# Kernel tuning notes

Hardware: AMD Instinct MI355X
Metric: run time of the kernel (lower is better)

The kernel has to match this reference:

```python
import jax, jax.numpy as jnp
import numpy as np
import math

B, S, D, H = 1, 2048, 2048, 16
DH = D // H  # 128
HALF = DH // 2  # 64


def setup_inputs() -> dict:
    key = jax.random.key(0)
    ks = jax.random.split(key, 6)
    x = jax.random.normal(ks[0], (B, S, D), dtype=jnp.float32)
    # rotary frequencies: freqs_cis = exp(i * t * theta), theta_j = 10000^{-2j/DH}
    inv_freq = 1.0 / (10000.0 ** (np.arange(0, DH, 2, dtype=np.float32) / DH))  # [HALF]
    t = np.arange(S, dtype=np.float32)
    angles = np.outer(t, inv_freq)  # [S, HALF]
    freqs_cos = jnp.asarray(np.cos(angles), dtype=jnp.float32)
    freqs_sin = jnp.asarray(np.sin(angles), dtype=jnp.float32)
    # additive causal mask [1,1,S,S]
    mask = jnp.triu(jnp.full((S, S), -1e9, dtype=jnp.float32), k=1)[None, None]
    scale = 0.02
    wq = jax.random.normal(ks[1], (D, D), dtype=jnp.float32) * scale
    wk = jax.random.normal(ks[2], (D, D), dtype=jnp.float32) * scale
    wv = jax.random.normal(ks[3], (D, D), dtype=jnp.float32) * scale
    wo = jax.random.normal(ks[4], (D, D), dtype=jnp.float32) * scale
    return {"x": x, "freqs_cos": freqs_cos, "freqs_sin": freqs_sin, "mask": mask,
            "wq": wq, "wk": wk, "wv": wv, "wo": wo, "start_pos": 0}


def _apply_rope(t, cos, sin):
    # t: [B,S,H,DH]; cos/sin: [S,HALF] broadcast as [1,S,1,HALF]
    tr = t.reshape(*t.shape[:-1], HALF, 2)
    even, odd = tr[..., 0], tr[..., 1]
    c = cos[None, :, None, :]
    s = sin[None, :, None, :]
    out_even = even * c - odd * s
    out_odd = even * s + odd * c
    return jnp.stack([out_even, out_odd], axis=-1).reshape(t.shape)


def reference(x, freqs_cos, freqs_sin, mask, wq, wk, wv, wo, start_pos):
    bsz, seqlen, _ = x.shape
    q = (x @ wq.T).reshape(bsz, seqlen, H, DH)
    k = (x @ wk.T).reshape(bsz, seqlen, H, DH)
    v = (x @ wv.T).reshape(bsz, seqlen, H, DH)
    q = _apply_rope(q, freqs_cos, freqs_sin)
    k = _apply_rope(k, freqs_cos, freqs_sin)
    q = q.transpose(0, 2, 1, 3)  # [B,H,S,DH]
    k = k.transpose(0, 2, 1, 3)
    v = v.transpose(0, 2, 1, 3)
    scores = jnp.einsum('bhqd,bhkd->bhqk', q, k) / math.sqrt(DH) + mask
    probs = jax.nn.softmax(scores, axis=-1)
    out = jnp.einsum('bhqk,bhkd->bhqd', probs, v)  # [B,H,S,DH]
    # faithful to original: transpose(2,3) then view(bsz, seqlen, dim)
    out = out.transpose(0, 1, 3, 2).reshape(bsz, seqlen, D)
    return out @ wo.T
```

## Files before the change

kernel.cpp:

```cpp
#include <hip/hip_runtime.h>

typedef unsigned short u16;
typedef unsigned int   u32;
typedef short  short8   __attribute__((ext_vector_type(8)));
typedef float  floatx4  __attribute__((ext_vector_type(4)));
typedef u16    ushortx2 __attribute__((ext_vector_type(2)));
typedef u16    ushortx4 __attribute__((ext_vector_type(4)));

__device__ __forceinline__ float bf2f(u16 u) {
  union { u32 i; float f; } v; v.i = ((u32)u) << 16; return v.f;
}
__device__ __forceinline__ u16 f2bf(float x) {
  union { float f; u32 i; } v; v.f = x;
  u32 r = v.i + 0x7FFFu + ((v.i >> 16) & 1u);
  return (u16)(r >> 16);
}

#if __has_builtin(__builtin_amdgcn_exp2f)
#define EXP2F(x) __builtin_amdgcn_exp2f(x)
#else
#define EXP2F(x) __exp2f(x)
#endif

#define GLOAD_LDS16(gptr, lptr)                                                   \
  __builtin_amdgcn_global_load_lds(                                               \
      (const __attribute__((address_space(1))) void*)(gptr),                      \
      (__attribute__((address_space(3))) void*)(lptr), 16, 0, 0)

__global__ __launch_bounds__(256) void cvt_all(
    const floatx4* __restrict__ x,  const floatx4* __restrict__ wq,
    const floatx4* __restrict__ wk, const floatx4* __restrict__ wv,
    const floatx4* __restrict__ wo,
    ushortx4* __restrict__ xb, ushortx4* __restrict__ wqkv,
    ushortx4* __restrict__ wob) {
  int i = blockIdx.x * 256 + threadIdx.x;
  const floatx4* in; ushortx4* out;
  switch (blockIdx.y) {
    case 0:  in = x;  out = xb; break;
    case 1:  in = wq; out = wqkv; break;
    case 2:  in = wk; out = wqkv + (size_t)1048576; break;
    case 3:  in = wv; out = wqkv + (size_t)2097152; break;
    default: in = wo; out = wob; break;
  }
  floatx4 v = in[i];
  ushortx4 o;
  o.x = f2bf(v.x); o.y = f2bf(v.y); o.z = f2bf(v.z); o.w = f2bf(v.w);
  out[i] = o;
}

__global__ __launch_bounds__(256) void gemm_bt(
    const u16* __restrict__ A, const u16* __restrict__ B, void* __restrict__ Cv,
    int M, int N, int K, int lda, int ldb, int ldc,
    long batchA, long batchB, long batchC, int outBF16) {
  const int m0 = blockIdx.y << 7;
  const int n0 = blockIdx.x << 7;

  A += (long)blockIdx.z * batchA;
  B += (long)blockIdx.z * batchB;
  const long cbase = (long)blockIdx.z * batchC;

  __shared__ __align__(16) u16 As[128][64];
  __shared__ __align__(16) u16 Bs[128][64];

  const int t = threadIdx.x;
  const int lane = t & 63;
  const int wave = t >> 6;
  const int wm = (wave >> 1) << 6;
  const int wn = (wave & 1) << 6;
  const int quad = lane >> 4;
  const int mrow = lane & 15;
  const int sw8 = mrow & 7;

  floatx4 acc[4][4] = {};

  const int srow = lane >> 3;
  const int gseg = (((lane & 7) ^ srow) << 3);
  const u16* gA = A + (long)(m0 + (wave << 5) + srow) * lda + gseg;
  const u16* gB = B + (long)(n0 + (wave << 5) + srow) * ldb + gseg;

  for (int k0 = 0; k0 < K; k0 += 64) {
    __syncthreads();
#pragma unroll
    for (int ii = 0; ii < 4; ii++) {
      GLOAD_LDS16(gA + k0 + (size_t)(ii << 3) * lda, &As[(wave << 5) + (ii << 3)][0]);
      GLOAD_LDS16(gB + k0 + (size_t)(ii << 3) * ldb, &Bs[(wave << 5) + (ii << 3)][0]);
    }
    __syncthreads();

#pragma unroll
    for (int kh = 0; kh < 2; kh++) {
      const int sidx = ((kh << 2) | quad) ^ sw8;
      short8 af[4], bfr[4];
#pragma unroll
      for (int i = 0; i < 4; i++)
        af[i] = *(const short8*)&As[wm + (i << 4) + mrow][sidx << 3];
#pragma unroll
      for (int j = 0; j < 4; j++)
        bfr[j] = *(const short8*)&Bs[wn + (j << 4) + mrow][sidx << 3];
#pragma unroll
      for (int i = 0; i < 4; i++)
#pragma unroll
        for (int j = 0; j < 4; j++)
          acc[i][j] = __builtin_amdgcn_mfma_f32_16x16x32_bf16(af[i], bfr[j], acc[i][j], 0, 0, 0);
    }
  }

#pragma unroll
  for (int i = 0; i < 4; i++) {
    int row0 = m0 + wm + (i << 4) + (quad << 2);
#pragma unroll
    for (int j = 0; j < 4; j++) {
      int col = n0 + wn + (j << 4) + mrow;
#pragma unroll
      for (int r = 0; r < 4; r++) {
        long idx = cbase + (long)(row0 + r) * ldc + col;
        float val = acc[i][j][r];
        if (outBF16) ((u16*)Cv)[idx] = f2bf(val);
        else         ((float*)Cv)[idx] = val;
      }
    }
  }
}

__global__ __launch_bounds__(256) void transpose_v(const u16* __restrict__ src,
                                                   u16* __restrict__ dst) {
  __shared__ u16 tile[64][68];
  const int d0 = blockIdx.x << 6;
  const int s0 = blockIdx.y << 6;
  const int tx = (threadIdx.x & 15) << 2;
  const int ty = threadIdx.x >> 4;
#pragma unroll
  for (int rr = 0; rr < 64; rr += 16) {
    ushortx4 v = *(const ushortx4*)(src + (size_t)(s0 + ty + rr) * 6144 + d0 + tx);
    *(ushortx4*)&tile[ty + rr][tx] = v;
  }
  __syncthreads();
#pragma unroll
  for (int rr = 0; rr < 64; rr += 16) {
    int r = ty + rr;
    ushortx4 o;
    o.x = tile[tx + 0][r]; o.y = tile[tx + 1][r];
    o.z = tile[tx + 2][r]; o.w = tile[tx + 3][r];
    *(ushortx4*)(dst + (size_t)(d0 + r) * 2048 + s0 + tx) = o;
  }
}

__global__ __launch_bounds__(256) void rope_qk(u16* __restrict__ qkv,
                                               const float* __restrict__ cs,
                                               const float* __restrict__ sn) {
  int idx = blockIdx.x * 256 + threadIdx.x;
  int p = idx & 63;
  int h = (idx >> 6) & 15;
  int s = idx >> 10;
  float c  = cs[(s << 6) | p];
  float si = sn[(s << 6) | p];
  float scale = blockIdx.y ? 1.0f : 0.12751743f;
  size_t off = (size_t)s * 6144 + (blockIdx.y ? 2048 : 0) + (h << 7) + (p << 1);
  ushortx2 eo = *(ushortx2*)(qkv + off);
  float e = bf2f(eo.x), o = bf2f(eo.y);
  ushortx2 r;
  r.x = f2bf((e * c - o * si) * scale);
  r.y = f2bf((e * si + o * c) * scale);
  *(ushortx2*)(qkv + off) = r;
}

__global__ __launch_bounds__(256, 2) void flash_attn(
    const u16* __restrict__ QKVp, const u16* __restrict__ VTp,
    u16* __restrict__ ATp) {
  const int r0id = (int)blockIdx.x + ((int)blockIdx.y << 5);
  const int h    = r0id & 15;
  const int qsub = 31 - (r0id >> 4);
  const int q0 = qsub << 6;
  const int ktmax = qsub >> 1;

  __shared__ __align__(16) u16 Ks[128][128];
  __shared__ __align__(16) u16 Vs[128][128];
  __shared__ __align__(16) u16 Ps[64][128];

  const int t = threadIdx.x;
  const int lane = t & 63;
  const int wave = t >> 6;
  const int quad = lane >> 4;
  const int mrow = lane & 15;
  const int sw   = mrow & 7;
  const int wmS = (wave & 1) << 5;
  const int wnS = (wave >> 1) << 6;
  const int wmV = (wave >> 1) << 6;
  const int wnP = (wave & 1) << 5;

  const int r4  = lane >> 4;
  const int seg = lane & 15;
  const int c0 = ((seg ^ r4) << 3);
  const int c4 = ((seg ^ (r4 + 4)) << 3);

  const u16* qbase = QKVp + (size_t)q0 * 6144 + (h << 7);
  const u16* kbase = QKVp + 2048 + (h << 7);
  const u16* vbase = VTp + (size_t)(h << 7) * 2048;

  short8 aq[2][4];
#pragma unroll
  for (int i = 0; i < 2; i++)
#pragma unroll
    for (int kk = 0; kk < 4; kk++)
      aq[i][kk] = *(const short8*)(qbase + (size_t)(wmS + (i << 4) + mrow) * 6144 +
                                   (kk << 5) + (quad << 3));

  const short8 ones = {0x3F80, 0x3F80, 0x3F80, 0x3F80,
                       0x3F80, 0x3F80, 0x3F80, 0x3F80};

  floatx4 Oa[4][2] = {};
  floatx4 Oa1[2] = {};

  const float C2 = 23.083120654223414f;

  for (int kt = 0; kt <= ktmax; kt++) {
    __syncthreads();
    {
      int rr0 = wave << 5;
#pragma unroll
      for (int ii = 0; ii < 8; ii++) {
        int rr = rr0 + (ii << 2);
        GLOAD_LDS16(kbase + (size_t)((kt << 7) + rr + r4) * 6144 + ((ii & 1) ? c4 : c0),
                    &Ks[rr][0]);
        GLOAD_LDS16(vbase + (size_t)(rr + r4) * 2048 + (kt << 7) + ((ii & 1) ? c4 : c0),
                    &Vs[rr][0]);
      }
    }
    __syncthreads();

    floatx4 sa[2][4] = {};
#pragma unroll
    for (int kk = 0; kk < 4; kk++) {
      short8 bk[4];
#pragma unroll
      for (int j = 0; j < 4; j++)
        bk[j] = *(const short8*)&Ks[wnS + (j << 4) + mrow][(((kk << 2) | quad) ^ sw) << 3];
#pragma unroll
      for (int i = 0; i < 2; i++)
#pragma unroll
        for (int j = 0; j < 4; j++)
          sa[i][j] = __builtin_amdgcn_mfma_f32_16x16x32_bf16(aq[i][kk], bk[j], sa[i][j], 0, 0, 0);
    }
    if (kt == ktmax) {
#pragma unroll
      for (int i = 0; i < 2; i++)
#pragma unroll
        for (int j = 0; j < 4; j++)
#pragma unroll
          for (int r = 0; r < 4; r++) {
            int ql = q0 + wmS + (i << 4) + (quad << 2) + r;
            int sl = (kt << 7) + wnS + (j << 4) + mrow;
            if (sl > ql) sa[i][j][r] = -1e30f;
          }
    }
#pragma unroll
    for (int i = 0; i < 2; i++)
#pragma unroll
      for (int j = 0; j < 4; j++)
#pragma unroll
        for (int r = 0; r < 4; r++) {
          int row = wmS + (i << 4) + (quad << 2) + r;
          int col = wnS + (j << 4) + mrow;
          Ps[row][((((col >> 3) ^ (row & 7)) << 3) | (col & 7))] =
              f2bf(EXP2F(sa[i][j][r] - C2));
        }
    __syncthreads();

#pragma unroll
    for (int kk = 0; kk < 4; kk++) {
      short8 av[4], bp[2];
#pragma unroll
      for (int i = 0; i < 4; i++)
        av[i] = *(const short8*)&Vs[wmV + (i << 4) + mrow][(((kk << 2) | quad) ^ sw) << 3];
#pragma unroll
      for (int j = 0; j < 2; j++)
        bp[j] = *(const short8*)&Ps[wnP + (j << 4) + mrow][(((kk << 2) | quad) ^ sw) << 3];
#pragma unroll
      for (int i = 0; i < 4; i++)
#pragma unroll
        for (int j = 0; j < 2; j++)
          Oa[i][j] = __builtin_amdgcn_mfma_f32_16x16x32_bf16(av[i], bp[j], Oa[i][j], 0, 0, 0);
#pragma unroll
      for (int j = 0; j < 2; j++)
        Oa1[j] = __builtin_amdgcn_mfma_f32_16x16x32_bf16(ones, bp[j], Oa1[j], 0, 0, 0);
    }
  }

  float linv[2];
#pragma unroll
  for (int j = 0; j < 2; j++) linv[j] = 1.f / Oa1[j][0];
#pragma unroll
  for (int i = 0; i < 4; i++) {
    int drow = (h << 7) + wmV + (i << 4) + (quad << 2);
#pragma unroll
    for (int j = 0; j < 2; j++) {
      int col = q0 + wnP + (j << 4) + mrow;
#pragma unroll
      for (int r = 0; r < 4; r++)
        ATp[(size_t)(drow + r) * 2048 + col] = f2bf(Oa[i][j][r] * linv[j]);
    }
  }
}

__global__ __launch_bounds__(256) void reduce2(const floatx4* __restrict__ a,
                                               const floatx4* __restrict__ b,
                                               floatx4* __restrict__ o) {
  int i = blockIdx.x * 256 + threadIdx.x;
  o[i] = a[i] + b[i];
}

extern "C" void kernel_launch(void* const* d_in, const int* in_sizes, int n_in,
                              void* d_out, int out_size, void* d_ws, size_t ws_size,
                              hipStream_t stream) {
  const float* x  = (const float*)d_in[0];
  const float* fc = (const float*)d_in[1];
  const float* fs = (const float*)d_in[2];
  const float* wq = (const float*)d_in[4];
  const float* wk = (const float*)d_in[5];
  const float* wv = (const float*)d_in[6];
  const float* wo = (const float*)d_in[7];
  float* out = (float*)d_out;

  char* ws = (char*)d_ws;
  const size_t MB = 1024 * 1024;
  u16*   XB   = (u16*)(ws + 0 * MB);
  u16*   WQKV = (u16*)(ws + 8 * MB);
  u16*   WOb  = (u16*)(ws + 32 * MB);
  u16*   QKV  = (u16*)(ws + 40 * MB);
  u16*   VT   = (u16*)(ws + 64 * MB);
  u16*   AT   = (u16*)(ws + 72 * MB);
  float* PART = (float*)(ws + 80 * MB);

  int use_split = (ws_size >= 113 * MB);

  dim3 blk(256);
  cvt_all<<<dim3(4096, 5), blk, 0, stream>>>(
      (const floatx4*)x, (const floatx4*)wq, (const floatx4*)wk,
      (const floatx4*)wv, (const floatx4*)wo,
      (ushortx4*)XB, (ushortx4*)WQKV, (ushortx4*)WOb);

  gemm_bt<<<dim3(48, 16, 1), blk, 0, stream>>>(XB, WQKV, QKV, 2048, 6144, 2048,
                                               2048, 2048, 6144, 0, 0, 0, 1);

  transpose_v<<<dim3(32, 32), blk, 0, stream>>>(QKV + 4096, VT);
  rope_qk<<<dim3(8192, 2), blk, 0, stream>>>(QKV, fc, fs);

  flash_attn<<<dim3(32, 16), blk, 0, stream>>>(QKV, VT, AT);

  if (use_split) {
    gemm_bt<<<dim3(16, 16, 2), blk, 0, stream>>>(AT, WOb, PART, 2048, 2048, 1024,
                                                 2048, 2048, 2048,
                                                 1024, 1024, (long)2048 * 2048, 0);
    reduce2<<<4096, blk, 0, stream>>>((const floatx4*)PART,
                                      (const floatx4*)(PART + (size_t)2048 * 2048),
                                      (floatx4*)out);
  } else {
    gemm_bt<<<dim3(16, 16, 1), blk, 0, stream>>>(AT, WOb, out, 2048, 2048, 2048,
                                                 2048, 2048, 2048, 0, 0, 0, 0);
  }
}
```

Baseline: 302.5 us.

## Shrink GEMM K-tile, fuse V transpose with RoPE, use atomic split-K output

The GEMM K-tile drops from 64 to 32 with a new LDS swizzle, which halves shared memory per block but doubles the number of barrier pairs. The V transpose and RoPE kernels merge into one launch. The output projection's split-K now writes its two partials by atomic add into a zeroed output, removing the partial buffer and the reduce kernel. Flash attention issues its V tile loads after a barrier that follows the K loads, reordering the loads relative to the K·Q compute.

```diff
diff --git a/kernel.cpp b/kernel.cpp
--- a/kernel.cpp
+++ b/kernel.cpp
@@ -51,7 +51,7 @@
 __global__ __launch_bounds__(256) void gemm_bt(
     const u16* __restrict__ A, const u16* __restrict__ B, void* __restrict__ Cv,
     int M, int N, int K, int lda, int ldb, int ldc,
-    long batchA, long batchB, long batchC, int outBF16) {
+    long batchA, long batchB, long batchC, int outMode) {
   const int m0 = blockIdx.y << 7;
   const int n0 = blockIdx.x << 7;
 
@@ -59,8 +59,8 @@
   B += (long)blockIdx.z * batchB;
   const long cbase = (long)blockIdx.z * batchC;
 
-  __shared__ __align__(16) u16 As[128][64];
-  __shared__ __align__(16) u16 Bs[128][64];
+  __shared__ __align__(16) u16 As[128][32];
+  __shared__ __align__(16) u16 Bs[128][32];
 
   const int t = threadIdx.x;
   const int lane = t & 63;
@@ -69,40 +69,40 @@
   const int wn = (wave & 1) << 6;
   const int quad = lane >> 4;
   const int mrow = lane & 15;
-  const int sw8 = mrow & 7;
 
   floatx4 acc[4][4] = {};
 
-  const int srow = lane >> 3;
-  const int gseg = (((lane & 7) ^ srow) << 3);
-  const u16* gA = A + (long)(m0 + (wave << 5) + srow) * lda + gseg;
-  const u16* gB = B + (long)(n0 + (wave << 5) + srow) * ldb + gseg;
-
-  for (int k0 = 0; k0 < K; k0 += 64) {
-    __syncthreads();
-#pragma unroll
-    for (int ii = 0; ii < 4; ii++) {
-      GLOAD_LDS16(gA + k0 + (size_t)(ii << 3) * lda, &As[(wave << 5) + (ii << 3)][0]);
-      GLOAD_LDS16(gB + k0 + (size_t)(ii << 3) * ldb, &Bs[(wave << 5) + (ii << 3)][0]);
-    }
-    __syncthreads();
-
-#pragma unroll
-    for (int kh = 0; kh < 2; kh++) {
-      const int sidx = ((kh << 2) | quad) ^ sw8;
-      short8 af[4], bfr[4];
-#pragma unroll
-      for (int i = 0; i < 4; i++)
-        af[i] = *(const short8*)&As[wm + (i << 4) + mrow][sidx << 3];
+  const int srow = (wave << 5) + (lane >> 2);
+  const int sseg = (((lane & 3) ^ ((lane >> 3) & 3)) << 3);
+  const u16* gA = A + (long)(m0 + srow) * lda + sseg;
+  const u16* gB = B + (long)(n0 + srow) * ldb + sseg;
+  u16* ldsA0 = &As[(wave << 5)][0];
+  u16* ldsA1 = &As[(wave << 5) + 16][0];
+  u16* ldsB0 = &Bs[(wave << 5)][0];
+  u16* ldsB1 = &Bs[(wave << 5) + 16][0];
+
+  const int qsw = ((quad ^ ((mrow >> 1) & 3)) << 3);
+
+  for (int k0 = 0; k0 < K; k0 += 32) {
+    __syncthreads();
+    GLOAD_LDS16(gA + k0,            ldsA0);
+    GLOAD_LDS16(gA + k0 + 16 * lda, ldsA1);
+    GLOAD_LDS16(gB + k0,            ldsB0);
+    GLOAD_LDS16(gB + k0 + 16 * ldb, ldsB1);
+    __syncthreads();
+
+    short8 af[4], bfr[4];
+#pragma unroll
+    for (int i = 0; i < 4; i++)
+      af[i] = *(const short8*)&As[wm + (i << 4) + mrow][qsw];
+#pragma unroll
+    for (int j = 0; j < 4; j++)
+      bfr[j] = *(const short8*)&Bs[wn + (j << 4) + mrow][qsw];
+#pragma unroll
+    for (int i = 0; i < 4; i++)
 #pragma unroll
       for (int j = 0; j < 4; j++)
-        bfr[j] = *(const short8*)&Bs[wn + (j << 4) + mrow][sidx << 3];
-#pragma unroll
-      for (int i = 0; i < 4; i++)
-#pragma unroll
-        for (int j = 0; j < 4; j++)
-          acc[i][j] = __builtin_amdgcn_mfma_f32_16x16x32_bf16(af[i], bfr[j], acc[i][j], 0, 0, 0);
-    }
+        acc[i][j] = __builtin_amdgcn_mfma_f32_16x16x32_bf16(af[i], bfr[j], acc[i][j], 0, 0, 0);
   }
 
 #pragma unroll
@@ -115,53 +115,58 @@
       for (int r = 0; r < 4; r++) {
         long idx = cbase + (long)(row0 + r) * ldc + col;
         float val = acc[i][j][r];
-        if (outBF16) ((u16*)Cv)[idx] = f2bf(val);
-        else         ((float*)Cv)[idx] = val;
+        if (outMode == 1)      ((u16*)Cv)[idx] = f2bf(val);
+        else if (outMode == 0) ((float*)Cv)[idx] = val;
+        else                   unsafeAtomicAdd(((float*)Cv) + idx, val);
       }
     }
   }
 }
 
-__global__ __launch_bounds__(256) void transpose_v(const u16* __restrict__ src,
-                                                   u16* __restrict__ dst) {
-  __shared__ u16 tile[64][68];
-  const int d0 = blockIdx.x << 6;
-  const int s0 = blockIdx.y << 6;
-  const int tx = (threadIdx.x & 15) << 2;
-  const int ty = threadIdx.x >> 4;
-#pragma unroll
-  for (int rr = 0; rr < 64; rr += 16) {
-    ushortx4 v = *(const ushortx4*)(src + (size_t)(s0 + ty + rr) * 6144 + d0 + tx);
-    *(ushortx4*)&tile[ty + rr][tx] = v;
-  }
-  __syncthreads();
-#pragma unroll
-  for (int rr = 0; rr < 64; rr += 16) {
-    int r = ty + rr;
-    ushortx4 o;
-    o.x = tile[tx + 0][r]; o.y = tile[tx + 1][r];
-    o.z = tile[tx + 2][r]; o.w = tile[tx + 3][r];
-    *(ushortx4*)(dst + (size_t)(d0 + r) * 2048 + s0 + tx) = o;
-  }
-}
-
-__global__ __launch_bounds__(256) void rope_qk(u16* __restrict__ qkv,
+__global__ __launch_bounds__(256) void prep_kv(u16* __restrict__ qkv,
+                                               u16* __restrict__ vt,
                                                const float* __restrict__ cs,
                                                const float* __restrict__ sn) {
-  int idx = blockIdx.x * 256 + threadIdx.x;
-  int p = idx & 63;
-  int h = (idx >> 6) & 15;
-  int s = idx >> 10;
-  float c  = cs[(s << 6) | p];
-  float si = sn[(s << 6) | p];
-  float scale = blockIdx.y ? 1.0f : 0.12751743f;
-  size_t off = (size_t)s * 6144 + (blockIdx.y ? 2048 : 0) + (h << 7) + (p << 1);
-  ushortx2 eo = *(ushortx2*)(qkv + off);
-  float e = bf2f(eo.x), o = bf2f(eo.y);
-  ushortx2 r;
-  r.x = f2bf((e * c - o * si) * scale);
-  r.y = f2bf((e * si + o * c) * scale);
-  *(ushortx2*)(qkv + off) = r;
+  const int b = blockIdx.x;
+  if (b < 1024) {
+    __shared__ u16 tile[64][68];
+    const int d0 = (b & 31) << 6;
+    const int s0 = (b >> 5) << 6;
+    const int tx = (threadIdx.x & 15) << 2;
+    const int ty = threadIdx.x >> 4;
+    const u16* src = qkv + 4096;
+#pragma unroll
+    for (int rr = 0; rr < 64; rr += 16) {
+      ushortx4 v = *(const ushortx4*)(src + (size_t)(s0 + ty + rr) * 6144 + d0 + tx);
+      *(ushortx4*)&tile[ty + rr][tx] = v;
+    }
+    __syncthreads();
+#pragma unroll
+    for (int rr = 0; rr < 64; rr += 16) {
+      int r = ty + rr;
+      ushortx4 o;
+      o.x = tile[tx + 0][r]; o.y = tile[tx + 1][r];
+      o.z = tile[tx + 2][r]; o.w = tile[tx + 3][r];
+      *(ushortx4*)(vt + (size_t)(d0 + r) * 2048 + s0 + tx) = o;
+    }
+  } else {
+    int idx = (b - 1024) * 256 + threadIdx.x;
+    int plane = idx >> 21;
+    idx &= (1 << 21) - 1;
+    int p = idx & 63;
+    int h = (idx >> 6) & 15;
+    int s = idx >> 10;
+    float c  = cs[(s << 6) | p];
+    float si = sn[(s << 6) | p];
+    float scale = plane ? 1.0f : 0.12751743f;
+    size_t off = (size_t)s * 6144 + (plane ? 2048 : 0) + (h << 7) + (p << 1);
+    ushortx2 eo = *(ushortx2*)(qkv + off);
+    float e = bf2f(eo.x), o = bf2f(eo.y);
+    ushortx2 r;
+    r.x = f2bf((e * c - o * si) * scale);
+    r.y = f2bf((e * si + o * c) * scale);
+    *(ushortx2*)(qkv + off) = r;
+  }
 }
 
 __global__ __launch_bounds__(256, 2) void flash_attn(
@@ -222,11 +227,18 @@
         int rr = rr0 + (ii << 2);
         GLOAD_LDS16(kbase + (size_t)((kt << 7) + rr + r4) * 6144 + ((ii & 1) ? c4 : c0),
                     &Ks[rr][0]);
+      }
+    }
+    __syncthreads();
+    {
+      int rr0 = wave << 5;
+#pragma unroll
+      for (int ii = 0; ii < 8; ii++) {
+        int rr = rr0 + (ii << 2);
         GLOAD_LDS16(vbase + (size_t)(rr + r4) * 2048 + (kt << 7) + ((ii & 1) ? c4 : c0),
                     &Vs[rr][0]);
       }
     }
-    __syncthreads();
 
     floatx4 sa[2][4] = {};
 #pragma unroll
@@ -300,13 +312,6 @@
         ATp[(size_t)(drow + r) * 2048 + col] = f2bf(Oa[i][j][r] * linv[j]);
     }
   }
-}
-
-__global__ __launch_bounds__(256) void reduce2(const floatx4* __restrict__ a,
-                                               const floatx4* __restrict__ b,
-                                               floatx4* __restrict__ o) {
-  int i = blockIdx.x * 256 + threadIdx.x;
-  o[i] = a[i] + b[i];
 }
 
 extern "C" void kernel_launch(void* const* d_in, const int* in_sizes, int n_in,
@@ -329,9 +334,6 @@
   u16*   QKV  = (u16*)(ws + 40 * MB);
   u16*   VT   = (u16*)(ws + 64 * MB);
   u16*   AT   = (u16*)(ws + 72 * MB);
-  float* PART = (float*)(ws + 80 * MB);
-
-  int use_split = (ws_size >= 113 * MB);
 
   dim3 blk(256);
   cvt_all<<<dim3(4096, 5), blk, 0, stream>>>(
@@ -342,20 +344,12 @@
   gemm_bt<<<dim3(48, 16, 1), blk, 0, stream>>>(XB, WQKV, QKV, 2048, 6144, 2048,
                                                2048, 2048, 6144, 0, 0, 0, 1);
 
-  transpose_v<<<dim3(32, 32), blk, 0, stream>>>(QKV + 4096, VT);
-  rope_qk<<<dim3(8192, 2), blk, 0, stream>>>(QKV, fc, fs);
+  prep_kv<<<17408, blk, 0, stream>>>(QKV, VT, fc, fs);
 
   flash_attn<<<dim3(32, 16), blk, 0, stream>>>(QKV, VT, AT);
 
-  if (use_split) {
-    gemm_bt<<<dim3(16, 16, 2), blk, 0, stream>>>(AT, WOb, PART, 2048, 2048, 1024,
-                                                 2048, 2048, 2048,
-                                                 1024, 1024, (long)2048 * 2048, 0);
-    reduce2<<<4096, blk, 0, stream>>>((const floatx4*)PART,
-                                      (const floatx4*)(PART + (size_t)2048 * 2048),
-                                      (floatx4*)out);
-  } else {
-    gemm_bt<<<dim3(16, 16, 1), blk, 0, stream>>>(AT, WOb, out, 2048, 2048, 2048,
-                                                 2048, 2048, 2048, 0, 0, 0, 0);
-  }
-}
+  hipMemsetAsync(out, 0, (size_t)out_size * sizeof(float), stream);
+  gemm_bt<<<dim3(16, 16, 2), blk, 0, stream>>>(AT, WOb, out, 2048, 2048, 1024,
+                                               2048, 2048, 2048,
+                                               1024, 1024, 0, 2);
+}
```

New measurement: 317.1 us. 4.8% more time.
